# Optimization experiments

Hardware: AMD Instinct MI355X
Metric: run time of the kernel (lower is better)

Reference implementation:

```python
import jax, jax.numpy as jnp
import numpy as np

B, NQ, NC, D, C = 8, 1024, 4096, 256, 24  # batch, n_query, n_context, emb_dim, num_classes


def setup_inputs() -> dict:
    key = jax.random.key(0)
    ks = jax.random.split(key, 11)
    sc = 0.05  # param init scale
    return {
        "q_head": jax.random.normal(ks[0], (B, NQ, D), jnp.float32),
        "q_tail": jax.random.normal(ks[1], (B, NQ, D), jnp.float32),
        "c_head": jax.random.normal(ks[2], (B, NC, D), jnp.float32),
        "c_tail": jax.random.normal(ks[3], (B, NC, D), jnp.float32),
        "context_labels": jax.random.randint(ks[4], (B, NC), 0, C + 1),
        "mask": jnp.ones((B, NC), jnp.float32),
        "W_rel": jax.random.normal(ks[5], (2 * D, D), jnp.float32) * sc,
        "b_rel": jnp.zeros((D,), jnp.float32),
        "W_gen": jax.random.normal(ks[6], (D, C + 1), jnp.float32) * sc,
        "b_gen": jnp.zeros((C + 1,), jnp.float32),
        "W_cp": jax.random.normal(ks[7], (2 * D, 1), jnp.float32) * sc,
        "b_cp": jnp.zeros((1,), jnp.float32),
    }


def reference(q_head, q_tail, c_head, c_tail, context_labels, mask,
              W_rel, b_rel, W_gen, b_gen, W_cp, b_cp):
    def rel_emb(h, t):
        return jnp.concatenate([h, t], axis=-1) @ W_rel + b_rel

    q_emb = rel_emb(q_head, q_tail)            # [B, NQ, D]
    c_emb = rel_emb(c_head, c_tail)            # [B, NC, D]

    # generate distribution
    gen_dist = jax.nn.log_softmax(q_emb @ W_gen + b_gen, axis=-1)  # [B, NQ, C+1]

    # attention distribution (copy)
    scores = jnp.einsum('bqd,bjd->bqj', q_emb, c_emb) * mask[:, None, :]  # [B, NQ, NC]
    lsm = jax.nn.log_softmax(scores, axis=-1)
    probs = jnp.exp(lsm)
    context_vec = jnp.einsum('bqj,bjd->bqd', probs, c_emb)  # [B, NQ, D]

    # grouped logsumexp over context labels == log(sum of softmax probs per class);
    # empty classes give log(0) = -inf, matching the original -inf mask + logsumexp.
    onehot = jax.nn.one_hot(context_labels, C + 1, dtype=probs.dtype)  # [B, NC, C+1]
    copy_dist = jnp.log(jnp.einsum('bqj,bjc->bqc', probs, onehot))     # [B, NQ, C+1]

    # should-copy gate
    logits = (jnp.concatenate([q_emb, context_vec], axis=-1) @ W_cp + b_cp)[..., 0]  # [B, NQ]
    copy_prob = jax.nn.log_sigmoid(logits)[..., None]
    gen_prob = jax.nn.log_sigmoid(-logits)[..., None]

    return jnp.logaddexp(copy_prob + copy_dist, gen_prob + gen_dist)  # [B, NQ, C+1]
```

## Files before the change

kernel.cpp:

```cpp
#include <hip/hip_runtime.h>


typedef __attribute__((ext_vector_type(8))) _Float16 half8;
typedef __attribute__((ext_vector_type(4))) float floatx4;

#define WB 8
#define WNQ 1024
#define WNC 4096
#define NROWS 8192

static __device__ __forceinline__ float logsig(float x) {
    return (x >= 0.f) ? -log1pf(__expf(-x)) : x - log1pf(__expf(x));
}

union V16h { int4 v; half8 h8; _Float16 h[8]; unsigned short s[8]; uint2 u2[2]; };
union F8   { float4 v[2]; float f[8]; };
union H4   { _Float16 h[4]; uint2 u; unsigned short s[4]; };

static __device__ __forceinline__ void async_lds16(const _Float16* g, _Float16* l) {
    __builtin_amdgcn_global_load_lds(
        (const __attribute__((address_space(1))) unsigned int*)g,
        (__attribute__((address_space(3))) unsigned int*)l,
        16, 0, 0);
}

static __device__ __forceinline__ void async_lds16f(const float* g, float* l) {
    __builtin_amdgcn_global_load_lds(
        (const __attribute__((address_space(1))) unsigned int*)g,
        (__attribute__((address_space(3))) unsigned int*)l,
        16, 0, 0);
}

__global__ void wprep_kernel(const float* __restrict__ Wrel,
                             const float* __restrict__ Wgen,
                             const float* __restrict__ Wcp,
                             _Float16* __restrict__ WT,
                             _Float16* __restrict__ GenB)
{
    const int bx = blockIdx.x;
    if (bx < 256) {
        const int n = bx;
        for (int k = threadIdx.x; k < 512; k += 256)
            WT[(long)n * 512 + k] = (_Float16)Wrel[(long)k * 256 + n];
    } else {
        const int n = bx - 256;
        const int k = threadIdx.x;
        float v = 0.f;
        if (n < 25)       v = Wgen[(long)k * 25 + n];
        else if (n == 25) v = Wcp[k];
        GenB[(long)n * 256 + k] = (_Float16)v;
    }
}

__global__ __launch_bounds__(256, 2) void emb_kernel(
    const float* __restrict__ q_head, const float* __restrict__ q_tail,
    const float* __restrict__ c_head, const float* __restrict__ c_tail,
    const _Float16* __restrict__ WT,
    const float* __restrict__ brel,
    const _Float16* __restrict__ GenB,
    const float* __restrict__ bgen,
    _Float16* __restrict__ Qf, _Float16* __restrict__ Cf,
    _Float16* __restrict__ CfT,
    float* __restrict__ genlog)
{
    __shared__ float sA32[2][2048];
    __shared__ _Float16 sO[64 * 264];

    const int tid  = threadIdx.x;
    const int lane = tid & 63;
    const int wv   = tid >> 6;
    const int l15  = lane & 15;
    const int quad = lane >> 4;
    const int n0   = wv * 64;

    const float* head; const float* tail; _Float16* Ef;
    long m0; bool isQ;
    if (blockIdx.x < 128) {
        isQ = true;  head = q_head; tail = q_tail; Ef = Qf;
        m0 = (long)blockIdx.x * 64;
    } else {
        isQ = false; head = c_head; tail = c_tail; Ef = Cf;
        m0 = (long)(blockIdx.x - 128) * 64;
    }

    const int srow = wv * 8 + (lane >> 3);
    const int sch  = lane & 7;

    auto stageA = [&](int kg, int buf) {
        const float* srcb = (kg < 256) ? (head + kg) : (tail + (kg - 256));
#pragma unroll
        for (int t = 0; t < 2; ++t) {
            const int r = t * 32 + srow;
            const int colsw = ((sch ^ (r & 7)) << 2);
            async_lds16f(srcb + (m0 + r) * 256 + colsw,
                         &sA32[buf][t * 1024 + wv * 256]);
        }
    };

    floatx4 acc[4][4];
#pragma unroll
    for (int a = 0; a < 4; ++a)
#pragma unroll
        for (int bq = 0; bq < 4; ++bq) acc[a][bq] = (floatx4)(0.0f);

    V16h wCur[4];
#pragma unroll
    for (int nt = 0; nt < 4; ++nt)
        wCur[nt].v = *(const int4*)(WT + (long)(n0 + nt * 16 + l15) * 512 + quad * 8);

    stageA(0, 0);

    for (int ks = 0; ks < 16; ++ks) {
        const int cur = ks & 1;
        __syncthreads();

        V16h wNxt[4];
        if (ks < 15) {
            const int kg = (ks + 1) * 32;
            stageA(kg, cur ^ 1);
#pragma unroll
            for (int nt = 0; nt < 4; ++nt)
                wNxt[nt].v = *(const int4*)(WT + (long)(n0 + nt * 16 + l15) * 512 + kg + quad * 8);
        } else {
#pragma unroll
            for (int nt = 0; nt < 4; ++nt) wNxt[nt] = wCur[nt];
        }

        V16h af[4];
#pragma unroll
        for (int mb = 0; mb < 4; ++mb) {
            const int row  = mb * 16 + l15;
            const int base = row * 32;
            const int p0   = ((quad * 2)     ^ (row & 7)) * 4;
            const int p1   = ((quad * 2 + 1) ^ (row & 7)) * 4;
            const float4 f0 = *(const float4*)&sA32[cur][base + p0];
            const float4 f1 = *(const float4*)&sA32[cur][base + p1];
            af[mb].h[0] = (_Float16)f0.x; af[mb].h[1] = (_Float16)f0.y;
            af[mb].h[2] = (_Float16)f0.z; af[mb].h[3] = (_Float16)f0.w;
            af[mb].h[4] = (_Float16)f1.x; af[mb].h[5] = (_Float16)f1.y;
            af[mb].h[6] = (_Float16)f1.z; af[mb].h[7] = (_Float16)f1.w;
        }
#pragma unroll
        for (int mb = 0; mb < 4; ++mb)
#pragma unroll
            for (int nt = 0; nt < 4; ++nt)
                acc[mb][nt] = __builtin_amdgcn_mfma_f32_16x16x32_f16(af[mb].h8, wCur[nt].h8, acc[mb][nt], 0, 0, 0);

#pragma unroll
        for (int nt = 0; nt < 4; ++nt) wCur[nt] = wNxt[nt];
    }

    float bias[4];
#pragma unroll
    for (int nt = 0; nt < 4; ++nt) bias[nt] = brel[n0 + nt * 16 + l15];

#pragma unroll
    for (int mb = 0; mb < 4; ++mb)
#pragma unroll
        for (int nt = 0; nt < 4; ++nt) {
            H4 hq;
#pragma unroll
            for (int r = 0; r < 4; ++r) {
                const long row = m0 + mb * 16 + quad * 4 + r;
                const _Float16 h = (_Float16)(acc[mb][nt][r] + bias[nt]);
                Ef[row * 256 + n0 + nt * 16 + l15] = h;
                hq.h[r] = h;
                if (isQ)
                    sO[(mb * 16 + quad * 4 + r) * 264 + n0 + nt * 16 + l15] = h;
            }
            if (!isQ) {
                const int n  = n0 + nt * 16 + l15;
                const int sw = (mb * 4 + quad) ^ l15;
                *(uint2*)&sO[n * 64 + sw * 4] = hq.u;
            }
        }

    __syncthreads();
    if (isQ) {
        floatx4 ga[2];
        ga[0] = (floatx4)(0.0f); ga[1] = (floatx4)(0.0f);
#pragma unroll
        for (int ks = 0; ks < 8; ++ks) {
            V16h a, b0, b1;
            a.v  = *(const int4*)&sO[(wv * 16 + l15) * 264 + ks * 32 + quad * 8];
            b0.v = *(const int4*)(GenB + (long)(l15)      * 256 + ks * 32 + quad * 8);
            b1.v = *(const int4*)(GenB + (long)(16 + l15) * 256 + ks * 32 + quad * 8);
            ga[0] = __builtin_amdgcn_mfma_f32_16x16x32_f16(a.h8, b0.h8, ga[0], 0, 0, 0);
            ga[1] = __builtin_amdgcn_mfma_f32_16x16x32_f16(a.h8, b1.h8, ga[1], 0, 0, 0);
        }
#pragma unroll
        for (int nt = 0; nt < 2; ++nt) {
            const int col = nt * 16 + l15;
            const float bb = (col < 25) ? bgen[col] : 0.f;
#pragma unroll
            for (int r = 0; r < 4; ++r)
                genlog[(m0 + wv * 16 + quad * 4 + r) * 32 + col] = ga[nt][r] + bb;
        }
    } else {
        const int bidx = (int)(m0 >> 12);
        const int jc0  = (int)(m0 & 4095);
        const int c    = tid & 7;
        const int nl   = tid >> 3;
#pragma unroll
        for (int i = 0; i < 8; ++i) {
            const int n  = nl + 32 * i;
            const int s0 = (2 * c)     ^ (n & 15);
            const int s1 = (2 * c + 1) ^ (n & 15);
            const uint2 u0 = *(const uint2*)&sO[n * 64 + s0 * 4];
            const uint2 u1 = *(const uint2*)&sO[n * 64 + s1 * 4];
            int4 out; out.x = u0.x; out.y = u0.y; out.z = u1.x; out.w = u1.y;
            *(int4*)&CfT[(long)bidx * 1048576 + (long)n * 4096 + jc0 + c * 8] = out;
        }
    }
}

__global__ __launch_bounds__(256, 2) void attn_kernel(
    const _Float16* __restrict__ qf,
    const _Float16* __restrict__ cf,
    const _Float16* __restrict__ cfT,
    const int*      __restrict__ labels,
    const float*    __restrict__ maskp,
    unsigned short* __restrict__ Oh,
    float* __restrict__ Mst,
    float* __restrict__ Lst,
    int jtiles, int nsh)
{
    __shared__ _Float16 sA[2][8192];
    __shared__ _Float16 sB[2][8192];
    __shared__ _Float16 Pw[4][16 * 40];

    const int tid  = threadIdx.x;
    const int lane = tid & 63;
    const int wv   = tid >> 6;
    const int l15  = lane & 15;
    const int quad = lane >> 4;

    const int f   = blockIdx.x;
    const int xcd = f & 7;
    const int seq = f >> 3;
    const int qt  = seq & 15;
    const int u   = seq >> 4;
    const int pr  = u * 8 + xcd;
    const int b   = pr >> nsh;
    const int sp  = pr & ((1 << nsh) - 1);
    const int q0  = qt * 64;

    V16h qfr[8];
    {
        const long qrow = (long)b * WNQ + q0 + wv * 16 + l15;
#pragma unroll
        for (int ks = 0; ks < 8; ++ks)
            qfr[ks].v = *(const int4*)(qf + qrow * 256 + ks * 32 + quad * 8);
    }

    floatx4 O[18];
#pragma unroll
    for (int i = 0; i < 18; ++i) O[i] = (floatx4)(0.0f);
    float m_run = -INFINITY;

    const int jb0 = sp * (jtiles * 32);

    const int spw = lane ^ ((lane >> 3) & 7);
    const int ddw = spw >> 2;
    const int jjw = spw & 3;

    auto stageTile = [&](int it, int buf) {
        const int jb = jb0 + it * 32;
        const long cbase = ((long)b * WNC + jb) * 256;
#pragma unroll
        for (int t = 0; t < 4; ++t) {
            const int idx = wv * 4 + t;
            const int ks = idx >> 1, jh = idx & 1;
            async_lds16(cf + cbase + (jh * 16 + l15) * 256 + ks * 32 + quad * 8,
                        &sA[buf][idx * 512]);
        }
        const long tbase = (long)b * 1048576 + jb;
#pragma unroll
        for (int t = 0; t < 4; ++t) {
            const int W = wv * 4 + t;
            async_lds16(cfT + tbase + (long)(W * 16 + ddw) * 4096 + jjw * 8,
                        &sB[buf][W * 512]);
        }
    };

    const int pvs   = 4 * l15 + quad;
    const int pvoff = (pvs ^ ((pvs >> 3) & 7)) * 8;

    stageTile(0, 0);

    for (int it = 0; it < jtiles; ++it) {
        const int cur = it & 1;
        const int jb  = jb0 + it * 32;

        __syncthreads();

        const float4 mv0 = *(const float4*)(maskp + (long)b * WNC + jb + quad * 4);
        const float4 mv1 = *(const float4*)(maskp + (long)b * WNC + jb + 16 + quad * 4);
        const int4   lb0 = *(const int4*)(labels + (long)b * WNC + jb + quad * 8);
        const int4   lb1 = *(const int4*)(labels + (long)b * WNC + jb + quad * 8 + 4);
        asm volatile("" ::: "memory");

        if (it + 1 < jtiles) stageTile(it + 1, cur ^ 1);

        floatx4 accS0 = (floatx4)(0.0f), accS1 = (floatx4)(0.0f);
        __builtin_amdgcn_s_setprio(1);
#pragma unroll
        for (int ks = 0; ks < 8; ++ks) {
            V16h a0, a1;
            a0.v = *(const int4*)&sA[cur][(ks * 2 + 0) * 512 + (quad * 16 + l15) * 8];
            a1.v = *(const int4*)&sA[cur][(ks * 2 + 1) * 512 + (quad * 16 + l15) * 8];
            accS0 = __builtin_amdgcn_mfma_f32_16x16x32_f16(a0.h8, qfr[ks].h8, accS0, 0, 0, 0);
            accS1 = __builtin_amdgcn_mfma_f32_16x16x32_f16(a1.h8, qfr[ks].h8, accS1, 0, 0, 0);
        }
        __builtin_amdgcn_s_setprio(0);
        const float* mv0p = (const float*)&mv0;
        const float* mv1p = (const float*)&mv1;
#pragma unroll
        for (int r = 0; r < 4; ++r) {
            accS0[r] *= mv0p[r];
            accS1[r] *= mv1p[r];
        }

        float v = fmaxf(fmaxf(fmaxf(accS0[0], accS0[1]), fmaxf(accS0[2], accS0[3])),
                        fmaxf(fmaxf(accS1[0], accS1[1]), fmaxf(accS1[2], accS1[3])));
        v = fmaxf(v, __shfl_xor(v, 16, 64));
        v = fmaxf(v, __shfl_xor(v, 32, 64));
        const float m_new = fmaxf(m_run, v);
        const bool upd = __any(m_new > m_run);
        const float alpha = __expf(m_run - m_new);
        float p[8];
#pragma unroll
        for (int r = 0; r < 4; ++r) {
            p[r]     = __expf(accS0[r] - m_new);
            p[4 + r] = __expf(accS1[r] - m_new);
        }
        m_run = m_new;

        if (upd) {
            float ar[4];
#pragma unroll
            for (int r = 0; r < 4; ++r) ar[r] = __shfl(alpha, quad * 4 + r, 64);
#pragma unroll
            for (int fo = 0; fo < 18; ++fo)
#pragma unroll
                for (int r = 0; r < 4; ++r) O[fo][r] *= ar[r];
        }

#pragma unroll
        for (int jf = 0; jf < 2; ++jf) {
            H4 w;
#pragma unroll
            for (int r = 0; r < 4; ++r) w.h[r] = (_Float16)p[jf * 4 + r];
            *(uint2*)&Pw[wv][l15 * 40 + jf * 16 + quad * 4] = w.u;
        }
        asm volatile("" ::: "memory");
        V16h pf;
        pf.v = *(const int4*)&Pw[wv][l15 * 40 + quad * 8];

        const int* lbp0 = (const int*)&lb0;
        const int* lbp1 = (const int*)&lb1;
        V16h oh0, oh1;
#pragma unroll
        for (int i = 0; i < 8; ++i) {
            const int lv = (i < 4) ? lbp0[i] : lbp1[i - 4];
            oh0.h[i] = (lv == l15)        ? (_Float16)1.0f : (_Float16)0.0f;
            oh1.h[i] = (lv == (l15 + 16) || l15 == 15) ? (_Float16)1.0f : (_Float16)0.0f;
        }

        __builtin_amdgcn_s_setprio(1);
#pragma unroll
        for (int dt = 0; dt < 16; ++dt) {
            V16h bfr;
            bfr.v = *(const int4*)&sB[cur][dt * 512 + pvoff];
            O[dt] = __builtin_amdgcn_mfma_f32_16x16x32_f16(pf.h8, bfr.h8, O[dt], 0, 0, 0);
        }
        O[16] = __builtin_amdgcn_mfma_f32_16x16x32_f16(pf.h8, oh0.h8, O[16], 0, 0, 0);
        O[17] = __builtin_amdgcn_mfma_f32_16x16x32_f16(pf.h8, oh1.h8, O[17], 0, 0, 0);
        __builtin_amdgcn_s_setprio(0);
    }

    {
        const long base = (long)(sp * WB + b) * WNQ + q0 + wv * 16;
#pragma unroll
        for (int dt = 0; dt < 18; ++dt)
#pragma unroll
            for (int r = 0; r < 4; ++r) {
                H4 h; h.h[0] = (_Float16)O[dt][r];
                Oh[(base + quad * 4 + r) * 288 + dt * 16 + l15] = h.s[0];
            }
        if (lane < 16) Mst[base + lane] = m_run;
        if (l15 == 15) {
#pragma unroll
            for (int r = 0; r < 4; ++r)
                Lst[base + quad * 4 + r] = O[17][r];
        }
    }
}

__global__ __launch_bounds__(256) void final_kernel(
    const float* __restrict__ genlog,
    const unsigned short* __restrict__ Oh,
    const float* __restrict__ Mst,
    const float* __restrict__ Lst,
    const float* __restrict__ Wcp,
    const float* __restrict__ bcp,
    float* __restrict__ outp,
    int ns)
{
    __shared__ float gA[4][32];
    __shared__ float cdA[4][32];

    const int tid  = threadIdx.x;
    const int lane = tid & 63;
    const int wv   = tid >> 6;
    const int row  = blockIdx.x * 4 + wv;

    float ms[8];
#pragma unroll
    for (int s = 0; s < 8; ++s) ms[s] = (s < ns) ? Mst[(long)s * NROWS + row] : -INFINITY;
    float mstar = -INFINITY;
#pragma unroll
    for (int s = 0; s < 8; ++s) mstar = fmaxf(mstar, ms[s]);
    float wgt[8]; float L = 0.f;
#pragma unroll
    for (int s = 0; s < 8; ++s) {
        wgt[s] = (ms[s] == -INFINITY) ? 0.f : __expf(ms[s] - mstar);
        if (s < ns) L += Lst[(long)s * NROWS + row] * wgt[s];
    }

    const int d0 = lane * 4;
    float ctx[4] = {0.f, 0.f, 0.f, 0.f};
#pragma unroll
    for (int s = 0; s < 8; ++s) {
        if (s < ns) {
            H4 t; t.u = *(const uint2*)&Oh[((long)s * NROWS + row) * 288 + d0];
#pragma unroll
            for (int i = 0; i < 4; ++i) ctx[i] += wgt[s] * (float)t.h[i];
        }
    }

    float cls[4] = {0.f, 0.f, 0.f, 0.f};
    if (lane < 8) {
#pragma unroll
        for (int s = 0; s < 8; ++s) {
            if (s < ns) {
                H4 t; t.u = *(const uint2*)&Oh[((long)s * NROWS + row) * 288 + 256 + lane * 4];
#pragma unroll
                for (int i = 0; i < 4; ++i) cls[i] += wgt[s] * (float)t.h[i];
            }
        }
    }

    float g = (lane < 25) ? genlog[(long)row * 32 + lane] : -INFINITY;
    float mg = g;
#pragma unroll
    for (int off = 32; off >= 1; off >>= 1) mg = fmaxf(mg, __shfl_xor(mg, off, 64));
    float se = (lane < 25) ? __expf(g - mg) : 0.f;
#pragma unroll
    for (int off = 32; off >= 1; off >>= 1) se += __shfl_xor(se, off, 64);
    const float glsm = g - mg - logf(se);

    const float qgate = genlog[(long)row * 32 + 25];
    const float invL = 1.f / L;
    float part = 0.f;
#pragma unroll
    for (int i = 0; i < 4; ++i)
        part += ctx[i] * invL * Wcp[256 + d0 + i];
#pragma unroll
    for (int off = 32; off >= 1; off >>= 1) part += __shfl_xor(part, off, 64);
    const float logit = qgate + part + bcp[0];

    const float lscp  = logsig(logit);
    const float lsgen = logsig(-logit);
    const float logL  = logf(L);

    if (lane < 8) {
#pragma unroll
        for (int i = 0; i < 4; ++i)
            cdA[wv][lane * 4 + i] = (cls[i] > 0.f) ? (logf(cls[i]) - logL) : -INFINITY;
    }
    if (lane < 25) gA[wv][lane] = glsm;
    __syncthreads();

    if (lane < 25) {
        const float a  = lscp + cdA[wv][lane];
        const float bb = lsgen + gA[wv][lane];
        const float mx = fmaxf(a, bb);
        const float o  = (mx == -INFINITY) ? -INFINITY
                         : mx + log1pf(__expf(fminf(a, bb) - mx));
        outp[(long)row * 25 + lane] = o;
    }
}

extern "C" void kernel_launch(void* const* d_in, const int* in_sizes, int n_in,
                              void* d_out, int out_size, void* d_ws, size_t ws_size,
                              hipStream_t stream) {
    const float* q_head = (const float*)d_in[0];
    const float* q_tail = (const float*)d_in[1];
    const float* c_head = (const float*)d_in[2];
    const float* c_tail = (const float*)d_in[3];
    const int*   labels = (const int*)d_in[4];
    const float* maskp  = (const float*)d_in[5];
    const float* Wrel   = (const float*)d_in[6];
    const float* brel   = (const float*)d_in[7];
    const float* Wgen   = (const float*)d_in[8];
    const float* bgen   = (const float*)d_in[9];
    const float* Wcp    = (const float*)d_in[10];
    const float* bcp    = (const float*)d_in[11];

    auto need = [](long ns) -> long { return 39075840l + ns * 4784128l; };
    int ns = 4, nsh = 2;
    if ((long)ws_size < need(4)) { ns = 2; nsh = 1; }
    if ((long)ws_size < need(2)) { ns = 1; nsh = 0; }
    const int jtiles = 128 / ns;

    char* ws = (char*)d_ws;
    _Float16* Qf     = (_Float16*)(ws);
    _Float16* Cf     = (_Float16*)(ws + 4194304l);
    _Float16* CfT    = (_Float16*)(ws + 20971520l);
    _Float16* WT     = (_Float16*)(ws + 37748736l);
    _Float16* GenB   = (_Float16*)(ws + 38010880l);
    float*    genlog = (float*)   (ws + 38027264l);
    unsigned short* Oh = (unsigned short*)(ws + 39075840l);
    float*    Mst    = (float*)   (ws + 39075840l + (long)ns * 4718592l);
    float*    Lst    = Mst + (long)ns * NROWS;

    hipLaunchKernelGGL(wprep_kernel, dim3(288), dim3(256), 0, stream,
                       Wrel, Wgen, Wcp, WT, GenB);
    hipLaunchKernelGGL(emb_kernel, dim3(640), dim3(256), 0, stream,
                       q_head, q_tail, c_head, c_tail, WT, brel, GenB, bgen,
                       Qf, Cf, CfT, genlog);
    hipLaunchKernelGGL(attn_kernel, dim3(16 * 8 * ns), dim3(256), 0, stream,
                       Qf, Cf, CfT, labels, maskp, Oh, Mst, Lst, jtiles, nsh);
    hipLaunchKernelGGL(final_kernel, dim3(NROWS / 4), dim3(256), 0, stream,
                       genlog, Oh, Mst, Lst, Wcp, bcp, (float*)d_out, ns);
}
```

Measured before the change: 249.0 us.

## Load context A-tile directly from global with register prefetch, raise occupancy and splits

Removes the sA shared-memory staging for the context tile used in the QK^T MFMA. Each wave now loads its A fragments straight from global memory into registers, software-prefetching the next k-slice (and the next tile's first slice) while the current MFMAs run. The freed LDS allows launch bounds of 3 blocks per SM, and the context split count rises to 8 when workspace permits, creating more blocks. In exchange, every wave reads the context rows from global/L2 without sharing across waves, and register pressure grows under the tighter occupancy bound.

New measurement: 402.8 us. +61.8%, slower.

```diff
diff --git a/kernel.cpp b/kernel.cpp
--- a/kernel.cpp
+++ b/kernel.cpp
@@ -214,7 +214,7 @@
     }
 }
 
-__global__ __launch_bounds__(256, 2) void attn_kernel(
+__global__ __launch_bounds__(256, 3) void attn_kernel(
     const _Float16* __restrict__ qf,
     const _Float16* __restrict__ cf,
     const _Float16* __restrict__ cfT,
@@ -225,7 +225,6 @@
     float* __restrict__ Lst,
     int jtiles, int nsh)
 {
-    __shared__ _Float16 sA[2][8192];
     __shared__ _Float16 sB[2][8192];
     __shared__ _Float16 Pw[4][16 * 40];
 
@@ -259,6 +258,10 @@
     float m_run = -INFINITY;
 
     const int jb0 = sp * (jtiles * 32);
+    const long cb0 = ((long)b * WNC + jb0) * 256;
+
+    const int ra0 = l15 * 256 + quad * 8;
+    const int ra1 = (16 + l15) * 256 + quad * 8;
 
     const int spw = lane ^ ((lane >> 3) & 7);
     const int ddw = spw >> 2;
@@ -266,14 +269,6 @@
 
     auto stageTile = [&](int it, int buf) {
         const int jb = jb0 + it * 32;
-        const long cbase = ((long)b * WNC + jb) * 256;
-#pragma unroll
-        for (int t = 0; t < 4; ++t) {
-            const int idx = wv * 4 + t;
-            const int ks = idx >> 1, jh = idx & 1;
-            async_lds16(cf + cbase + (jh * 16 + l15) * 256 + ks * 32 + quad * 8,
-                        &sA[buf][idx * 512]);
-        }
         const long tbase = (long)b * 1048576 + jb;
 #pragma unroll
         for (int t = 0; t < 4; ++t) {
@@ -286,13 +281,37 @@
     const int pvs   = 4 * l15 + quad;
     const int pvoff = (pvs ^ ((pvs >> 3) & 7)) * 8;
 
+    V16h pA0, pA1;
+    pA0.v = *(const int4*)(cf + cb0 + ra0);
+    pA1.v = *(const int4*)(cf + cb0 + ra1);
     stageTile(0, 0);
 
     for (int it = 0; it < jtiles; ++it) {
         const int cur = it & 1;
         const int jb  = jb0 + it * 32;
+        const _Float16* cq = cf + cb0 + (long)it * 8192;
 
         __syncthreads();
+
+        floatx4 accS0 = (floatx4)(0.0f), accS1 = (floatx4)(0.0f);
+        V16h a0c = pA0, a1c = pA1;
+        __builtin_amdgcn_s_setprio(1);
+#pragma unroll
+        for (int ks = 0; ks < 8; ++ks) {
+            V16h a0n, a1n;
+            if (ks < 7) {
+                a0n.v = *(const int4*)(cq + ra0 + (ks + 1) * 32);
+                a1n.v = *(const int4*)(cq + ra1 + (ks + 1) * 32);
+            } else if (it + 1 < jtiles) {
+                a0n.v = *(const int4*)(cq + 8192 + ra0);
+                a1n.v = *(const int4*)(cq + 8192 + ra1);
+            } else { a0n = a0c; a1n = a1c; }
+            accS0 = __builtin_amdgcn_mfma_f32_16x16x32_f16(a0c.h8, qfr[ks].h8, accS0, 0, 0, 0);
+            accS1 = __builtin_amdgcn_mfma_f32_16x16x32_f16(a1c.h8, qfr[ks].h8, accS1, 0, 0, 0);
+            a0c = a0n; a1c = a1n;
+        }
+        __builtin_amdgcn_s_setprio(0);
+        pA0 = a0c; pA1 = a1c;
 
         const float4 mv0 = *(const float4*)(maskp + (long)b * WNC + jb + quad * 4);
         const float4 mv1 = *(const float4*)(maskp + (long)b * WNC + jb + 16 + quad * 4);
@@ -302,17 +321,6 @@
 
         if (it + 1 < jtiles) stageTile(it + 1, cur ^ 1);
 
-        floatx4 accS0 = (floatx4)(0.0f), accS1 = (floatx4)(0.0f);
-        __builtin_amdgcn_s_setprio(1);
-#pragma unroll
-        for (int ks = 0; ks < 8; ++ks) {
-            V16h a0, a1;
-            a0.v = *(const int4*)&sA[cur][(ks * 2 + 0) * 512 + (quad * 16 + l15) * 8];
-            a1.v = *(const int4*)&sA[cur][(ks * 2 + 1) * 512 + (quad * 16 + l15) * 8];
-            accS0 = __builtin_amdgcn_mfma_f32_16x16x32_f16(a0.h8, qfr[ks].h8, accS0, 0, 0, 0);
-            accS1 = __builtin_amdgcn_mfma_f32_16x16x32_f16(a1.h8, qfr[ks].h8, accS1, 0, 0, 0);
-        }
-        __builtin_amdgcn_s_setprio(0);
         const float* mv0p = (const float*)&mv0;
         const float* mv1p = (const float*)&mv1;
 #pragma unroll
@@ -509,7 +517,8 @@
     const float* bcp    = (const float*)d_in[11];
 
     auto need = [](long ns) -> long { return 39075840l + ns * 4784128l; };
-    int ns = 4, nsh = 2;
+    int ns = 8, nsh = 3;
+    if ((long)ws_size < need(8)) { ns = 4; nsh = 2; }
     if ((long)ws_size < need(4)) { ns = 2; nsh = 1; }
     if ((long)ws_size < need(2)) { ns = 1; nsh = 0; }
     const int jtiles = 128 / ns;
```
